# Performance work log

Measured on AMD Instinct MI355X. Metric: run time of the kernel, lower is better.

Reference implementation:

```python
import jax, jax.numpy as jnp
import numpy as np

B, T, F = 256, 192, 8
CARD0, CARD1 = 1000, 100
E0, E1 = 32, 16
H = 512
D_IN = F + E0 + E1  # 56


def _glorot(key, shape):
    fan_in, fan_out = shape[0], shape[-1]
    lim = jnp.sqrt(6.0 / (fan_in + fan_out))
    return jax.random.uniform(key, shape, jnp.float32, -lim, lim)


def setup_inputs() -> dict:
    key = jax.random.key(0)
    ks = jax.random.split(key, 16)
    return {
        "x_cont": jax.random.normal(ks[0], (B, T, F), jnp.float32),
        "cat0": jax.random.randint(ks[1], (B, T), 0, CARD0),
        "cat1": jax.random.randint(ks[2], (B, T), 0, CARD1),
        "emb0": _glorot(ks[3], (CARD0, E0)),
        "emb1": _glorot(ks[4], (CARD1, E1)),
        "Wk1": _glorot(ks[5], (D_IN, 4 * H)),
        "Wr1": _glorot(ks[6], (H, 4 * H)),
        "b1": jnp.zeros((4 * H,), jnp.float32).at[H:2 * H].set(1.0),  # unit_forget_bias
        "Wk2": _glorot(ks[7], (H, 4 * H)),
        "Wr2": _glorot(ks[8], (H, 4 * H)),
        "b2": jnp.zeros((4 * H,), jnp.float32).at[H:2 * H].set(1.0),
        "Wmu": _glorot(ks[9], (H, 1)),
        "bmu": _glorot(ks[10], (1, 1))[0],
        "Wsig": _glorot(ks[11], (H, 1)),
        "bsig": _glorot(ks[12], (1, 1))[0],
    }


def _lstm(x, Wk, Wr, b):
    # x: [B, T, D]; Keras gate order i, f, g(c), o; zero initial states (inference mode,
    # dropout/recurrent_dropout inactive when training=False).
    xz = jnp.einsum('btd,dk->btk', x, Wk) + b  # precompute input projection for all steps
    h0 = jnp.zeros((x.shape[0], H), x.dtype)

    def step(carry, z_t):
        h, c = carry
        z = z_t + h @ Wr  # [B, 4H]
        i, f, g, o = jnp.split(z, 4, axis=-1)
        i = jax.nn.sigmoid(i)
        f = jax.nn.sigmoid(f)
        g = jnp.tanh(g)
        o = jax.nn.sigmoid(o)
        c = f * c + i * g
        h = o * jnp.tanh(c)
        return (h, c), h

    _, hs = jax.lax.scan(step, (h0, h0), jnp.swapaxes(xz, 0, 1))  # [T, B, H]
    return jnp.swapaxes(hs, 0, 1)


def reference(x_cont, cat0, cat1, emb0, emb1, Wk1, Wr1, b1, Wk2, Wr2, b2, Wmu, bmu, Wsig, bsig):
    x = jnp.concatenate([x_cont, emb0[cat0], emb1[cat1]], axis=-1)  # [B, T, 56]
    x = _lstm(x, Wk1, Wr1, b1)
    x = _lstm(x, Wk2, Wr2, b2)
    mu = x @ Wmu + bmu                      # count_data=False -> raw mu
    sigma = jax.nn.softplus(x @ Wsig + bsig)
    return (mu, sigma)
```

## Files before the change

### kernel.cpp

```cpp
#include <hip/hip_runtime.h>
#include <math.h>

#define Bsz 256
#define Tsz 192
#define Fc 8
#define E0c 32
#define E1c 16
#define Hc 512
#define G4 2048
#define DINP 64
#define K1t 576
#define K2t 1024
#define NBLK 256
#define KPAD1 584
#define KPAD2 1032
#define LDSB_BYTES (64 * KPAD2 * 2)
#define SLOT_STRIDE 16
#define RING_U (64 * SLOT_STRIDE)
#define WD_WAIT (1 << 17)

typedef __attribute__((ext_vector_type(8))) short short8;
typedef __attribute__((ext_vector_type(4))) float f32x4;

template<int N> struct IC { static constexpr int v = N; };
template<int C, int CMAX, typename F>
__device__ __forceinline__ void static_for(F&& f) {
    if constexpr (C < CMAX) {
        f(IC<C>{});
        static_for<C + 1, CMAX>(f);
    }
}

static __device__ __forceinline__ float bf2f(ushort u) {
    return __uint_as_float(((uint)u) << 16);
}
static __device__ __forceinline__ ushort f2bf(float f) {
    uint u = __float_as_uint(f);
    u = (u + 0x7fffu + ((u >> 16) & 1u)) >> 16;
    return (ushort)u;
}

static __device__ __forceinline__ float sigm_f(float x) {
    return __builtin_amdgcn_rcpf(1.f + __expf(-x));
}
static __device__ __forceinline__ float tanh_f(float x) {
    return 1.f - 2.f * __builtin_amdgcn_rcpf(1.f + __expf(2.f * x));
}

static __device__ __forceinline__ uint poll_sc1(const uint* p) {
    uint v;
    asm volatile("global_load_dword %0, %1, off sc1\n\t"
                 "s_waitcnt vmcnt(0)"
                 : "=v"(v) : "v"((unsigned long long)p) : "memory");
    return v;
}
static __device__ __forceinline__ void store_slot_sc1(uint* p, uint v) {
    asm volatile("global_store_dword %0, %1, off sc1"
                 :: "v"((unsigned long long)p), "v"(v) : "memory");
}

__global__ __launch_bounds__(256) void build_x_kernel(
    const float* __restrict__ x_cont, const int* __restrict__ cat0,
    const int* __restrict__ cat1, const float* __restrict__ emb0,
    const float* __restrict__ emb1, ushort* __restrict__ x_bf)
{
    int idx = blockIdx.x * 256 + threadIdx.x;
    if (idx >= Tsz * Bsz * DINP) return;
    int d = idx & 63;
    int row = idx >> 6;
    int t = row >> 8;
    int b = row & 255;
    float v = 0.f;
    if (d < Fc)                  v = x_cont[(b * Tsz + t) * Fc + d];
    else if (d < Fc + E0c)       v = emb0[cat0[b * Tsz + t] * E0c + (d - Fc)];
    else if (d < Fc + E0c + E1c) v = emb1[cat1[b * Tsz + t] * E1c + (d - Fc - E0c)];
    x_bf[idx] = f2bf(v);
}

__global__ __launch_bounds__(256) void transpose_w_kernel(
    const float* __restrict__ in, ushort* __restrict__ out, int K, int ldout, int coff)
{
    __shared__ float tile[32][33];
    int k0 = blockIdx.x * 32;
    int n0 = blockIdx.y * 32;
    int tx = threadIdx.x & 31, ty = threadIdx.x >> 5;
    #pragma unroll
    for (int p = 0; p < 4; ++p) {
        int k = k0 + ty + p * 8;
        tile[ty + p * 8][tx] = (k < K) ? in[k * G4 + n0 + tx] : 0.f;
    }
    __syncthreads();
    #pragma unroll
    for (int p = 0; p < 4; ++p) {
        int nl = ty + p * 8;
        out[(size_t)(n0 + nl) * ldout + coff + k0 + tx] = f2bf(tile[tx][nl]);
    }
}

static __device__ __forceinline__ uint poll_mask(const uint* arr, uint tg) {
    uint v = poll_sc1(arr + (threadIdx.x & 31) * SLOT_STRIDE);
    unsigned long long bal = __ballot((int)(v >= tg));
    return (uint)bal;
}
static __device__ __forceinline__ void wait_mask(const uint* arr, uint tg, uint need) {
    int it = 0;
    while ((poll_mask(arr, tg) & need) != need) {
        if (++it >= WD_WAIT) break;
        __builtin_amdgcn_s_sleep(1);
    }
}
static __device__ __forceinline__ void wait_all(const uint* arr, uint tg) {
    wait_mask(arr, tg, 0xFFFFFFFFu);
}

template<int C0, int C1, int KOFF, int KPADv>
static __device__ __forceinline__ void load_mfma_range(
    const ushort* p, const ushort* B_lds, int lane15, int quad, f32x4* acc)
{
    uint4 buf[C1 - C0];
    static_for<C0, C1>([&](auto Kc) {
        constexpr int ks = decltype(Kc)::v;
        buf[ks - C0] = *(const uint4*)(p + ks * 32);
    });
    asm volatile("" ::: "memory");
    static_for<C0, C1>([&](auto Kc) {
        constexpr int ks = decltype(Kc)::v;
        short8 av = __builtin_bit_cast(short8, buf[ks - C0]);
        #pragma unroll
        for (int gt = 0; gt < 4; ++gt) {
            short8 bfr = *(const short8*)&B_lds[(gt * 16 + lane15) * KPADv
                                               + (KOFF + ks) * 32 + quad * 8];
            acc[gt] = __builtin_amdgcn_mfma_f32_16x16x32_bf16(av, bfr, acc[gt], 0, 0, 0);
        }
    });
}

template<int KOFF, int KPADv>
static __device__ __forceinline__ void gated_phase16(
    const ushort* p, const uint* arr, uint tg,
    const ushort* B_lds, int lane15, int quad, f32x4* acc)
{
    uint m = poll_mask(arr, tg);
    if (m == 0xFFFFFFFFu) {
        load_mfma_range<0, 16, KOFF, KPADv>(p, B_lds, lane15, quad, acc);
    } else {
        wait_mask(arr, tg, 0x0000FFFFu);
        load_mfma_range<0, 8, KOFF, KPADv>(p, B_lds, lane15, quad, acc);
        wait_mask(arr, tg, 0xFFFF0000u);
        load_mfma_range<8, 16, KOFF, KPADv>(p, B_lds, lane15, quad, acc);
    }
}

template<int KS_IN, int KS_TOT, int LDA_IN, int KPADv, bool HAS_DEP, int FANOUT>
static __device__ __forceinline__ void run_layer(
    const ushort* __restrict__ Ain,
    ushort* __restrict__ hbuf,
    const ushort* __restrict__ hz,
    const ushort* __restrict__ Wt,
    const float* __restrict__ bias,
    ushort* B_lds,
    uint* pflags,
    int g, int jb, int m0, int j0)
{
    constexpr int KS_R = KS_TOT - KS_IN;
    constexpr int KL = KS_TOT * 32;
    constexpr int SEGS = KL / 8;
    int tid = threadIdx.x;
    int lane = tid & 63, wv = tid >> 6;
    int lane15 = lane & 15, quad = lane >> 4;
    int bid = jb * 8 + g * 2 + (HAS_DEP ? 1 : 0);

    uint* ring = pflags + (size_t)(bid * 4 + wv) * RING_U;
    const uint* own_arr = ring;
    const uint* dep_arr = ring + 32 * SLOT_STRIDE;

    uint* pub_dst;
    {
        int j = lane & 31;
        int cons_role = HAS_DEP ? 1 : (lane >> 5);
        int cons_bid = j * 8 + g * 2 + cons_role;
        pub_dst = pflags + (size_t)(cons_bid * 4 + wv) * RING_U
                + ((lane >= 32) ? 32 * SLOT_STRIDE : 0) + jb * SLOT_STRIDE;
    }

    for (int i = tid; i < 64 * SEGS; i += 256) {
        int row = i / SEGS, seg = i - row * SEGS;
        int gz = (row >> 4) * Hc + j0 + (row & 15);
        *(uint4*)&B_lds[row * KPADv + seg * 8] =
            *(const uint4*)(Wt + (size_t)gz * KL + seg * 8);
    }
    __syncthreads();

    float bgate[4];
    #pragma unroll
    for (int gt = 0; gt < 4; ++gt) bgate[gt] = bias[gt * Hc + j0 + lane15];
    float cst[4] = {0.f, 0.f, 0.f, 0.f};

    int arow = m0 + wv * 16 + lane15;
    int crow0 = m0 + wv * 16 + quad * 4;

    for (int t = 0; t < Tsz; ++t) {
        f32x4 acc[4];
        #pragma unroll
        for (int gt = 0; gt < 4; ++gt) acc[gt] = (f32x4){0.f, 0.f, 0.f, 0.f};

        {
            const ushort* p0 = Ain + ((size_t)t * Bsz + arow) * LDA_IN + quad * 8;
            if constexpr (HAS_DEP) {
                gated_phase16<0, KPADv>(p0, dep_arr, (uint)(t + 1),
                                        B_lds, lane15, quad, acc);
            } else {
                load_mfma_range<0, KS_IN, 0, KPADv>(p0, B_lds, lane15, quad, acc);
            }
        }

        {
            if (t == 0) {
                const ushort* p1 = hz + (size_t)arow * Hc + quad * 8;
                load_mfma_range<0, KS_R, KS_IN, KPADv>(p1, B_lds, lane15, quad, acc);
            } else {
                const ushort* p1 = hbuf + ((size_t)(t - 1) * Bsz + arow) * Hc + quad * 8;
                gated_phase16<KS_IN, KPADv>(p1, own_arr, (uint)t,
                                            B_lds, lane15, quad, acc);
            }
        }

        uint hv[4];
        #pragma unroll
        for (int r = 0; r < 4; ++r) {
            float zi = acc[0][r] + bgate[0];
            float zf = acc[1][r] + bgate[1];
            float zg = acc[2][r] + bgate[2];
            float zo = acc[3][r] + bgate[3];
            float ig = sigm_f(zi);
            float fg = sigm_f(zf);
            float gg = tanh_f(zg);
            float og = sigm_f(zo);
            float cn = fg * cst[r] + ig * gg;
            cst[r] = cn;
            float hn = og * tanh_f(cn);
            hv[r] = (uint)f2bf(hn);
        }
        {
            unsigned long long hb = (unsigned long long)
                &hbuf[((size_t)t * Bsz + crow0) * Hc + j0 + lane15];
            asm volatile(
                "global_store_short %0, %1, off sc1\n\t"
                "global_store_short %0, %2, off offset:1024 sc1\n\t"
                "global_store_short %0, %3, off offset:2048 sc1\n\t"
                "global_store_short %0, %4, off offset:3072 sc1\n\t"
                "s_waitcnt vmcnt(0)"
                :: "v"(hb), "v"(hv[0]), "v"(hv[1]), "v"(hv[2]), "v"(hv[3])
                : "memory");
        }
        if (lane < FANOUT)
            store_slot_sc1(pub_dst, (uint)(t + 1));
    }
}

__global__ __launch_bounds__(256, 1) void deepar_persistent(
    const ushort* __restrict__ x_bf,
    const ushort* __restrict__ Wt1, const ushort* __restrict__ Wt2,
    const float* __restrict__ b1, const float* __restrict__ b2,
    ushort* __restrict__ h1, ushort* __restrict__ h2,
    const ushort* __restrict__ hz,
    const float* __restrict__ Wmu, const float* __restrict__ bmu,
    const float* __restrict__ Wsig, const float* __restrict__ bsig,
    float* __restrict__ out, uint* __restrict__ pflags)
{
    extern __shared__ ushort B_lds[];

    int bid = blockIdx.x;
    int xcd = bid & 7;
    int g = xcd >> 1;
    int role = xcd & 1;
    int jb = bid >> 3;
    int m0 = g * 64;
    int j0 = jb * 16;

    if (role == 0) {
        run_layer<2, 18, DINP, KPAD1, false, 64>(x_bf, h1, hz, Wt1, b1, B_lds,
                                                 pflags, g, jb, m0, j0);
        return;
    }
    run_layer<16, 32, Hc, KPAD2, true, 32>(h1, h2, hz, Wt2, b2, B_lds,
                                           pflags, g, jb, m0, j0);

    {
        int wv = threadIdx.x >> 6;
        const uint* ring = pflags + (size_t)(bid * 4 + wv) * RING_U;
        wait_all(ring, (uint)Tsz);
    }
    __syncthreads();

    int lane = threadIdx.x & 63, wv = threadIdx.x >> 6;
    float wm[8], wsg[8];
    #pragma unroll
    for (int i = 0; i < 8; ++i) {
        wm[i] = Wmu[lane * 8 + i];
        wsg[i] = Wsig[lane * 8 + i];
    }
    float bmu0 = bmu[0], bsg0 = bsig[0];
    for (int i = jb * 4 + wv; i < 64 * Tsz; i += 128) {
        int b = m0 + (i & 63);
        int t = i >> 6;
        const ushort* hp = h2 + ((size_t)t * Bsz + b) * Hc + lane * 8;
        short8 hvv = *(const short8*)hp;
        float smu = 0.f, ssg = 0.f;
        #pragma unroll
        for (int e = 0; e < 8; ++e) {
            float f = bf2f((ushort)hvv[e]);
            smu += f * wm[e];
            ssg += f * wsg[e];
        }
        #pragma unroll
        for (int off = 32; off > 0; off >>= 1) {
            smu += __shfl_down(smu, off, 64);
            ssg += __shfl_down(ssg, off, 64);
        }
        if (lane == 0) {
            int oi = b * Tsz + t;
            float sg = ssg + bsg0;
            float sp = sg > 0.f ? sg + log1pf(__expf(-sg)) : log1pf(__expf(sg));
            out[oi] = smu + bmu0;
            out[Bsz * Tsz + oi] = sp;
        }
    }
}

extern "C" void kernel_launch(void* const* d_in, const int* in_sizes, int n_in,
                              void* d_out, int out_size, void* d_ws, size_t ws_size,
                              hipStream_t stream) {
    const float* x_cont = (const float*)d_in[0];
    const int*   cat0   = (const int*)d_in[1];
    const int*   cat1   = (const int*)d_in[2];
    const float* emb0   = (const float*)d_in[3];
    const float* emb1   = (const float*)d_in[4];
    const float* Wk1    = (const float*)d_in[5];
    const float* Wr1    = (const float*)d_in[6];
    const float* b1     = (const float*)d_in[7];
    const float* Wk2    = (const float*)d_in[8];
    const float* Wr2    = (const float*)d_in[9];
    const float* b2     = (const float*)d_in[10];
    const float* Wmu    = (const float*)d_in[11];
    const float* bmu    = (const float*)d_in[12];
    const float* Wsig   = (const float*)d_in[13];
    const float* bsig   = (const float*)d_in[14];
    float* out = (float*)d_out;

    const size_t pflags_bytes = (size_t)NBLK * 4 * RING_U * 4;

    char* ws = (char*)d_ws;
    uint*   pflags = (uint*)ws;                                ws += pflags_bytes;
    ushort* x_bf  = (ushort*)ws;                               ws += (size_t)Tsz * Bsz * DINP * 2;
    ushort* Wt1   = (ushort*)ws;                               ws += (size_t)G4 * K1t * 2;
    ushort* Wt2   = (ushort*)ws;                               ws += (size_t)G4 * K2t * 2;
    ushort* h1    = (ushort*)ws;                               ws += (size_t)Tsz * Bsz * Hc * 2;
    ushort* h2    = (ushort*)ws;                               ws += (size_t)Tsz * Bsz * Hc * 2;
    ushort* hz    = (ushort*)ws;                               ws += (size_t)Bsz * Hc * 2;

    hipMemsetAsync(pflags, 0, pflags_bytes, stream);
    hipMemsetAsync(hz, 0, (size_t)Bsz * Hc * 2, stream);

    build_x_kernel<<<(Tsz * Bsz * DINP + 255) / 256, 256, 0, stream>>>(
        x_cont, cat0, cat1, emb0, emb1, x_bf);
    transpose_w_kernel<<<dim3(2, 64), 256, 0, stream>>>(Wk1, Wt1, 56, K1t, 0);
    transpose_w_kernel<<<dim3(16, 64), 256, 0, stream>>>(Wr1, Wt1, Hc, K1t, DINP);
    transpose_w_kernel<<<dim3(16, 64), 256, 0, stream>>>(Wk2, Wt2, Hc, K2t, 0);
    transpose_w_kernel<<<dim3(16, 64), 256, 0, stream>>>(Wr2, Wt2, Hc, K2t, Hc);

    hipFuncSetAttribute((const void*)deepar_persistent,
                        hipFuncAttributeMaxDynamicSharedMemorySize, LDSB_BYTES);
    deepar_persistent<<<dim3(NBLK), dim3(256), LDSB_BYTES, stream>>>(
        x_bf, Wt1, Wt2, b1, b2, h1, h2, hz, Wmu, bmu, Wsig, bsig, out, pflags);
}
```

Before: 1.195 ms.

## Speculatively load hidden state and detect readiness via sentinel values

The h1/h2 buffers are pre-filled with 0xFFFF sentinels. Consumers now issue the 16 hidden-state loads straight away, with sc1 cache bypass, and check the data for sentinel bf16 values, skipping the flag polling when nothing is missing. When a sentinel is found it falls back to the flag-gated two-half load path. This takes the flag-poll round trip off the critical path of each timestep. In exchange it adds two large memsets of the h buffers per call, and a real bf16 NaN with pattern 0xFFFF would force the fallback path, which is still correct, just slower.

```diff
diff --git a/kernel.cpp b/kernel.cpp
--- a/kernel.cpp
+++ b/kernel.cpp
@@ -21,6 +21,7 @@
 
 typedef __attribute__((ext_vector_type(8))) short short8;
 typedef __attribute__((ext_vector_type(4))) float f32x4;
+typedef __attribute__((ext_vector_type(4))) uint u32x4;
 
 template<int N> struct IC { static constexpr int v = N; };
 template<int C, int CMAX, typename F>
@@ -57,6 +58,15 @@
 static __device__ __forceinline__ void store_slot_sc1(uint* p, uint v) {
     asm volatile("global_store_dword %0, %1, off sc1"
                  :: "v"((unsigned long long)p), "v"(v) : "memory");
+}
+static __device__ __forceinline__ u32x4 ld128_sc1(const void* p) {
+    u32x4 r;
+    asm volatile("global_load_dwordx4 %0, %1, off sc1"
+                 : "=v"(r) : "v"((unsigned long long)p));
+    return r;
+}
+static __device__ __forceinline__ uint sent2(uint u) {
+    return (uint)(((u & 0xFFFFu) == 0xFFFFu) | ((u >> 16) == 0xFFFFu));
 }
 
 __global__ __launch_bounds__(256) void build_x_kernel(
@@ -113,19 +123,21 @@
     wait_mask(arr, tg, 0xFFFFFFFFu);
 }
 
-template<int C0, int C1, int KOFF, int KPADv>
-static __device__ __forceinline__ void load_mfma_range(
-    const ushort* p, const ushort* B_lds, int lane15, int quad, f32x4* acc)
-{
-    uint4 buf[C1 - C0];
+template<int C0, int C1>
+static __device__ __forceinline__ void issue_sc1(const ushort* p, u32x4* buf) {
     static_for<C0, C1>([&](auto Kc) {
         constexpr int ks = decltype(Kc)::v;
-        buf[ks - C0] = *(const uint4*)(p + ks * 32);
+        buf[ks] = ld128_sc1(p + ks * 32);
     });
-    asm volatile("" ::: "memory");
+}
+
+template<int C0, int C1, int KOFF, int KPADv>
+static __device__ __forceinline__ void mfma_range(
+    const u32x4* buf, const ushort* B_lds, int lane15, int quad, f32x4* acc)
+{
     static_for<C0, C1>([&](auto Kc) {
         constexpr int ks = decltype(Kc)::v;
-        short8 av = __builtin_bit_cast(short8, buf[ks - C0]);
+        short8 av = __builtin_bit_cast(short8, buf[ks]);
         #pragma unroll
         for (int gt = 0; gt < 4; ++gt) {
             short8 bfr = *(const short8*)&B_lds[(gt * 16 + lane15) * KPADv
@@ -135,20 +147,49 @@
     });
 }
 
+template<int C0, int C1, int KOFF, int KPADv>
+static __device__ __forceinline__ void load_mfma_plain(
+    const ushort* p, const ushort* B_lds, int lane15, int quad, f32x4* acc)
+{
+    u32x4 buf[16];
+    static_for<C0, C1>([&](auto Kc) {
+        constexpr int ks = decltype(Kc)::v;
+        buf[ks] = __builtin_bit_cast(u32x4, *(const uint4*)(p + ks * 32));
+    });
+    asm volatile("" ::: "memory");
+    mfma_range<C0, C1, KOFF, KPADv>(buf, B_lds, lane15, quad, acc);
+}
+
 template<int KOFF, int KPADv>
-static __device__ __forceinline__ void gated_phase16(
+static __device__ __forceinline__ void gated_phase16_spec(
     const ushort* p, const uint* arr, uint tg,
     const ushort* B_lds, int lane15, int quad, f32x4* acc)
 {
-    uint m = poll_mask(arr, tg);
-    if (m == 0xFFFFFFFFu) {
-        load_mfma_range<0, 16, KOFF, KPADv>(p, B_lds, lane15, quad, acc);
-    } else {
-        wait_mask(arr, tg, 0x0000FFFFu);
-        load_mfma_range<0, 8, KOFF, KPADv>(p, B_lds, lane15, quad, acc);
-        wait_mask(arr, tg, 0xFFFF0000u);
-        load_mfma_range<8, 16, KOFF, KPADv>(p, B_lds, lane15, quad, acc);
-    }
+    u32x4 buf[16];
+    issue_sc1<0, 16>(p, buf);
+    asm volatile("s_waitcnt vmcnt(0)" ::: "memory");
+    __builtin_amdgcn_sched_barrier(0);
+    uint bad = 0;
+    static_for<0, 16>([&](auto Kc) {
+        constexpr int ks = decltype(Kc)::v;
+        u32x4 b = buf[ks];
+        #pragma unroll
+        for (int d = 0; d < 4; ++d) bad |= sent2(b[d]);
+    });
+    if (!__any((int)bad)) {
+        mfma_range<0, 16, KOFF, KPADv>(buf, B_lds, lane15, quad, acc);
+        return;
+    }
+    wait_mask(arr, tg, 0x0000FFFFu);
+    issue_sc1<0, 8>(p, buf);
+    asm volatile("s_waitcnt vmcnt(0)" ::: "memory");
+    __builtin_amdgcn_sched_barrier(0);
+    mfma_range<0, 8, KOFF, KPADv>(buf, B_lds, lane15, quad, acc);
+    wait_mask(arr, tg, 0xFFFF0000u);
+    issue_sc1<8, 16>(p, buf);
+    asm volatile("s_waitcnt vmcnt(0)" ::: "memory");
+    __builtin_amdgcn_sched_barrier(0);
+    mfma_range<8, 16, KOFF, KPADv>(buf, B_lds, lane15, quad, acc);
 }
 
 template<int KS_IN, int KS_TOT, int LDA_IN, int KPADv, bool HAS_DEP, int FANOUT>
@@ -207,21 +248,21 @@
         {
             const ushort* p0 = Ain + ((size_t)t * Bsz + arow) * LDA_IN + quad * 8;
             if constexpr (HAS_DEP) {
-                gated_phase16<0, KPADv>(p0, dep_arr, (uint)(t + 1),
-                                        B_lds, lane15, quad, acc);
+                gated_phase16_spec<0, KPADv>(p0, dep_arr, (uint)(t + 1),
+                                             B_lds, lane15, quad, acc);
             } else {
-                load_mfma_range<0, KS_IN, 0, KPADv>(p0, B_lds, lane15, quad, acc);
+                load_mfma_plain<0, KS_IN, 0, KPADv>(p0, B_lds, lane15, quad, acc);
             }
         }
 
         {
             if (t == 0) {
                 const ushort* p1 = hz + (size_t)arow * Hc + quad * 8;
-                load_mfma_range<0, KS_R, KS_IN, KPADv>(p1, B_lds, lane15, quad, acc);
+                load_mfma_plain<0, KS_R, KS_IN, KPADv>(p1, B_lds, lane15, quad, acc);
             } else {
                 const ushort* p1 = hbuf + ((size_t)(t - 1) * Bsz + arow) * Hc + quad * 8;
-                gated_phase16<KS_IN, KPADv>(p1, own_arr, (uint)t,
-                                            B_lds, lane15, quad, acc);
+                gated_phase16_spec<KS_IN, KPADv>(p1, own_arr, (uint)t,
+                                                 B_lds, lane15, quad, acc);
             }
         }
 
@@ -305,7 +346,10 @@
         int b = m0 + (i & 63);
         int t = i >> 6;
         const ushort* hp = h2 + ((size_t)t * Bsz + b) * Hc + lane * 8;
-        short8 hvv = *(const short8*)hp;
+        u32x4 rv = ld128_sc1(hp);
+        asm volatile("s_waitcnt vmcnt(0)" ::: "memory");
+        __builtin_amdgcn_sched_barrier(0);
+        short8 hvv = __builtin_bit_cast(short8, rv);
         float smu = 0.f, ssg = 0.f;
         #pragma unroll
         for (int e = 0; e < 8; ++e) {
@@ -349,17 +393,20 @@
     float* out = (float*)d_out;
 
     const size_t pflags_bytes = (size_t)NBLK * 4 * RING_U * 4;
+    const size_t h_bytes = (size_t)Tsz * Bsz * Hc * 2;
 
     char* ws = (char*)d_ws;
     uint*   pflags = (uint*)ws;                                ws += pflags_bytes;
     ushort* x_bf  = (ushort*)ws;                               ws += (size_t)Tsz * Bsz * DINP * 2;
     ushort* Wt1   = (ushort*)ws;                               ws += (size_t)G4 * K1t * 2;
     ushort* Wt2   = (ushort*)ws;                               ws += (size_t)G4 * K2t * 2;
-    ushort* h1    = (ushort*)ws;                               ws += (size_t)Tsz * Bsz * Hc * 2;
-    ushort* h2    = (ushort*)ws;                               ws += (size_t)Tsz * Bsz * Hc * 2;
+    ushort* h1    = (ushort*)ws;                               ws += h_bytes;
+    ushort* h2    = (ushort*)ws;                               ws += h_bytes;
     ushort* hz    = (ushort*)ws;                               ws += (size_t)Bsz * Hc * 2;
 
     hipMemsetAsync(pflags, 0, pflags_bytes, stream);
+    hipMemsetAsync(h1, 0xFF, h_bytes, stream);
+    hipMemsetAsync(h2, 0xFF, h_bytes, stream);
     hipMemsetAsync(hz, 0, (size_t)Bsz * Hc * 2, stream);
 
     build_x_kernel<<<(Tsz * Bsz * DINP + 255) / 256, 256, 0, stream>>>(
```

After: 1.777 ms. 48.7% more time.
